# Optimization experiments

Measured on AMD Instinct MI355X. Metric: run time of the kernel, lower is better.

Reference implementation:

```python
import jax, jax.numpy as jnp
import numpy as np
from jax import lax

P = 2048
HIDDEN = 512
NUM_STEPS = 15
BATCH = 8192
SLOPE = 25.0  # snntorch surrogate.fast_sigmoid default slope


@jax.custom_vjp
def spike_fn(x):
    # Heaviside forward, fast-sigmoid surrogate backward.
    return (x > 0).astype(x.dtype)

def _spike_fwd(x):
    return spike_fn(x), x

def _spike_bwd(x, g):
    return (g / (SLOPE * jnp.abs(x) + 1.0) ** 2,)

spike_fn.defvjp(_spike_fwd, _spike_bwd)


def setup_inputs() -> dict:
    key = jax.random.key(0)
    ks = jax.random.split(key, 6)
    x = jax.random.randint(ks[0], (BATCH, 2), 0, P)
    embed = jax.random.normal(ks[1], (P, HIDDEN), dtype=jnp.float32)
    # Linear weights stored [in, out] (transpose of torch convention, same math)
    W1 = jax.random.normal(ks[2], (2 * HIDDEN, HIDDEN), dtype=jnp.float32) * (1.0 / np.sqrt(2 * HIDDEN))
    b1 = jnp.zeros((HIDDEN,), dtype=jnp.float32)
    W2 = jax.random.normal(ks[3], (HIDDEN, P), dtype=jnp.float32) * (1.0 / np.sqrt(HIDDEN))
    b2 = jnp.zeros((P,), dtype=jnp.float32)
    beta1 = jnp.float32(0.9)
    thr1 = jnp.float32(1.0)
    beta2 = jnp.float32(0.9)
    thr2 = jnp.float32(1.0)
    return {"x": x, "embed": embed, "W1": W1, "b1": b1, "W2": W2, "b2": b2,
            "beta1": beta1, "thr1": thr1, "beta2": beta2, "thr2": thr2}


def reference(x, embed, W1, b1, W2, b2, beta1, thr1, beta2, thr2):
    # clamp params as in the torch no-grad block (identity at init values)
    beta1 = jnp.clip(beta1, 0.1, 0.9)
    beta2 = jnp.clip(beta2, 0.1, 0.9)
    thr1 = jnp.clip(thr1, 0.1, None)
    thr2 = jnp.clip(thr2, 0.1, None)

    emb = embed[x].reshape(x.shape[0], -1)          # [B, 2*hidden]
    cur1 = emb @ W1 + b1                            # constant across steps

    mem1_0 = jnp.zeros((x.shape[0], HIDDEN), dtype=jnp.float32)
    mem2_0 = jnp.zeros((x.shape[0], P), dtype=jnp.float32)

    def step(carry, _):
        mem1, mem2 = carry
        # snntorch Leaky, reset_mechanism='subtract': reset from PREVIOUS mem, detached
        reset1 = lax.stop_gradient((mem1 - thr1 > 0).astype(mem1.dtype))
        mem1 = beta1 * mem1 + cur1 - reset1 * thr1
        spk1 = spike_fn(mem1 - thr1)
        cur2 = spk1 @ W2 + b2
        # lif2 has reset_mechanism='none'
        mem2 = beta2 * mem2 + cur2
        return (mem1, mem2), None

    (mem1, mem2), _ = lax.scan(step, (mem1_0, mem2_0), None, length=NUM_STEPS)
    return mem2  # output = last mem2
```

## Files before the change

### kernel.cpp

```cpp
#include <hip/hip_runtime.h>
#include <hip/hip_bf16.h>
#include <stdint.h>

typedef float    f32x4 __attribute__((ext_vector_type(4)));
typedef _Float16 f16x4 __attribute__((ext_vector_type(4)));
typedef _Float16 f16x8 __attribute__((ext_vector_type(8)));

#define NSTEPS 15

__global__ __launch_bounds__(256) void prep_kernel(
    const float* __restrict__ embed, const float* __restrict__ W1,
    const float* __restrict__ W2,
    _Float16* __restrict__ Ap, _Float16* __restrict__ Btp,
    _Float16* __restrict__ W2T)
{
  __shared__ _Float16 sh[2][64][72];
  const int b = blockIdx.x;
  const int t = threadIdx.x;

  if (b < 1024) {
    const int i  = b * 256 + t;
    const int m  = i >> 7;
    const int k4 = (i & 127) * 4;
    f32x4 v = *(const f32x4*)&embed[(size_t)m * 512 + k4];
    f16x4 h0, h1;
#pragma unroll
    for (int j = 0; j < 4; ++j) {
      h0[j] = (_Float16)v[j];
      h1[j] = (_Float16)(v[j] - (float)h0[j]);
    }
    _Float16* r = Ap + (size_t)m * 1024 + k4;
    *(f16x4*)(r)       = h0;
    *(f16x4*)(r + 512) = h1;
  } else if (b < 1152) {
    const int idx = b - 1024;
    const int n0 = (idx & 7) * 64;
    const int k0 = ((idx >> 3) & 7) * 64;
    const int z  = idx >> 6;
    const int kk = t >> 4;
    const int n4 = (t & 15) * 4;
#pragma unroll
    for (int i = 0; i < 4; ++i) {
      f32x4 v = *(const f32x4*)&W1[(size_t)(z * 512 + k0 + kk + i * 16) * 512 + n0 + n4];
#pragma unroll
      for (int j = 0; j < 4; ++j) {
        float s = v[j] * 64.0f;
        _Float16 hi = (_Float16)s;
        sh[0][n4 + j][kk + i * 16] = hi;
        sh[1][n4 + j][kk + i * 16] = (_Float16)(s - (float)hi);
      }
    }
    __syncthreads();
#pragma unroll
    for (int i = 0; i < 2; ++i) {
      const int nn = (t >> 3) + i * 32;
      const int k8 = (t & 7) * 8;
      _Float16* r = Btp + (size_t)(z * 512 + n0 + nn) * 1024 + k0 + k8;
      *(uint4*)(r)       = *(const uint4*)&sh[0][nn][k8];
      *(uint4*)(r + 512) = *(const uint4*)&sh[1][nn][k8];
    }
  } else {
    const int idx = b - 1152;
    const int n0 = (idx & 31) * 64;
    const int k0 = (idx >> 5) * 64;
    const int kk = t >> 4;
    const int n4 = (t & 15) * 4;
#pragma unroll
    for (int i = 0; i < 4; ++i) {
      f32x4 v = *(const f32x4*)&W2[(size_t)(k0 + kk + i * 16) * 2048 + n0 + n4];
#pragma unroll
      for (int j = 0; j < 4; ++j) sh[0][n4 + j][kk + i * 16] = (_Float16)v[j];
    }
    __syncthreads();
#pragma unroll
    for (int i = 0; i < 2; ++i) {
      const int nn = (t >> 3) + i * 32;
      const int k8 = (t & 7) * 8;
      *(uint4*)&W2T[(size_t)(n0 + nn) * 512 + k0 + k8] = *(const uint4*)&sh[0][nn][k8];
    }
  }
}

__device__ __forceinline__ void gld_lds16(const void* g, void* l) {
  __builtin_amdgcn_global_load_lds(
      (const __attribute__((address_space(1))) uint32_t*)g,
      (__attribute__((address_space(3))) uint32_t*)l, 16, 0, 0);
}

__global__ __launch_bounds__(256) void gemm1_kernel(
    const _Float16* __restrict__ Ap,
    const _Float16* __restrict__ Btp,
    float* __restrict__ T)
{
  __shared__ __align__(16) char lds[16384];
  char* AsB = lds;
  char* BsB = lds + 8192;

  const int t    = threadIdx.x;
  const int lane = t & 63;
  const int wave = t >> 6;
  const int wm   = wave >> 1;
  const int wn   = wave & 1;

  int bid = blockIdx.x;
  bid = (bid & 7) * 64 + (bid >> 3);
  const int m0 = (bid >> 4) * 64;
  const int n0 = (bid & 15) * 64;

  f32x4 acc[2][2] = {};

  for (int kt = 0; kt < 24; ++kt) {
    const int vk0  = kt * 64;
    const int acol = (vk0 < 1024) ? vk0 : vk0 - 1024;
    const int bcol = (vk0 < 1024) ? (vk0 & 511) : vk0 - 512;
#pragma unroll
    for (int i = 0; i < 2; ++i) {
      const int ob  = (wave * 2 + i) * 1024;
      const int o   = ob + lane * 16;
      const int row = o >> 7;
      const int c   = ((o >> 4) & 7) ^ (row & 7);
      gld_lds16(Ap + ((size_t)(m0 + row) * 1024 + acol + c * 8), AsB + ob);
    }
#pragma unroll
    for (int i = 0; i < 2; ++i) {
      const int ob  = (wave * 2 + i) * 1024;
      const int o   = ob + lane * 16;
      const int row = o >> 7;
      const int c   = ((o >> 4) & 7) ^ (row & 7);
      gld_lds16(Btp + ((size_t)(n0 + row) * 1024 + bcol + c * 8), BsB + ob);
    }
    asm volatile("s_waitcnt vmcnt(0)" ::: "memory");
    __syncthreads();

#pragma unroll
    for (int kk = 0; kk < 2; ++kk) {
      const int lc = (lane >> 4) + kk * 4;
      f16x8 af[2], bf[2];
#pragma unroll
      for (int mi = 0; mi < 2; ++mi) {
        const int row = wm * 32 + mi * 16 + (lane & 15);
        af[mi] = *(const f16x8*)(AsB + row * 128 + ((lc ^ (row & 7)) << 4));
      }
#pragma unroll
      for (int ni = 0; ni < 2; ++ni) {
        const int row = wn * 32 + ni * 16 + (lane & 15);
        bf[ni] = *(const f16x8*)(BsB + row * 128 + ((lc ^ (row & 7)) << 4));
      }
#pragma unroll
      for (int mi = 0; mi < 2; ++mi)
#pragma unroll
        for (int ni = 0; ni < 2; ++ni)
          acc[mi][ni] = __builtin_amdgcn_mfma_f32_16x16x32_f16(
              af[mi], bf[ni], acc[mi][ni], 0, 0, 0);
    }
    __syncthreads();
  }

#pragma unroll
  for (int mi = 0; mi < 2; ++mi) {
    const int r0 = m0 + wm * 32 + mi * 16 + ((lane >> 4) << 2);
#pragma unroll
    for (int ni = 0; ni < 2; ++ni) {
      const int cc = n0 + wn * 32 + ni * 16 + (lane & 15);
#pragma unroll
      for (int q = 0; q < 4; ++q)
        T[(size_t)(r0 + q) * 1024 + cc] = acc[mi][ni][q] * 0.015625f;
    }
  }
}

__global__ __launch_bounds__(256) void recur_kernel(
    const int* __restrict__ x,
    const float* __restrict__ T,
    const float* __restrict__ b1,
    const float* __restrict__ beta1p, const float* __restrict__ thr1p,
    const float* __restrict__ beta2p,
    _Float16* __restrict__ S)
{
  const float beta1 = fminf(fmaxf(beta1p[0], 0.1f), 0.9f);
  const float thr1  = fmaxf(thr1p[0], 0.1f);
  const float beta2 = fminf(fmaxf(beta2p[0], 0.1f), 0.9f);

  const int t = threadIdx.x;
  const int b = blockIdx.x * 4 + (t >> 6);
  const int h = (t & 63) * 8;
  const int x0 = x[b * 2 + 0];
  const int x1 = x[b * 2 + 1];

  const float* p0 = &T[(size_t)x0 * 1024 + h];
  const float* p1 = &T[(size_t)x1 * 1024 + 512 + h];

  float cur[8];
#pragma unroll
  for (int half = 0; half < 2; ++half) {
    f32x4 a = *(const f32x4*)(p0 + half * 4);
    f32x4 c = *(const f32x4*)(p1 + half * 4);
    f32x4 e = *(const f32x4*)&b1[h + half * 4];
#pragma unroll
    for (int j = 0; j < 4; ++j)
      cur[half * 4 + j] = (a[j] + c[j]) + e[j];
  }

  float m[8] = {}, s[8] = {};
#pragma unroll
  for (int st = 0; st < NSTEPS; ++st) {
#pragma unroll
    for (int j = 0; j < 8; ++j) {
      float r = (m[j] > thr1) ? thr1 : 0.0f;
      m[j] = beta1 * m[j] + cur[j] - r;
      float sp = (m[j] > thr1) ? 1.0f : 0.0f;
      s[j] = beta2 * s[j] + sp;
    }
  }

  __align__(16) _Float16 o[8];
#pragma unroll
  for (int j = 0; j < 8; ++j) o[j] = (_Float16)s[j];
  *(uint4*)&S[(size_t)b * 512 + h] = *(const uint4*)o;
}

__device__ __forceinline__ void g2_round(
    const _Float16* __restrict__ A, const _Float16* __restrict__ Bt,
    char* lds, int m0, int n0, int wave, int lane, int tile, int r)
{
  const int k0 = tile * 64;
  char* lb = lds + (tile % 3) * 49152;
  if (r < 4) {
    const int ob  = r * 8192 + wave * 1024;
    const int o   = ob + lane * 16;
    const int row = o >> 7;
    const int c   = ((o >> 4) & 7) ^ (row & 7);
    gld_lds16(A + ((size_t)(m0 + row) * 512 + k0 + c * 8), lb + ob);
  } else {
    const int ob  = (r - 4) * 8192 + wave * 1024;
    const int o   = ob + lane * 16;
    const int row = o >> 7;
    const int c   = ((o >> 4) & 7) ^ (row & 7);
    gld_lds16(Bt + ((size_t)(n0 + row) * 512 + k0 + c * 8), lb + 32768 + ob);
  }
}

template<int QA>
__device__ __forceinline__ void g2_mfma16(
    f32x4 (&acc)[8][2], const f16x8 (&af)[4][2], const f16x8 (&bf)[2][2])
{
#pragma unroll
  for (int kk = 0; kk < 2; ++kk)
#pragma unroll
    for (int mi = 0; mi < 4; ++mi)
#pragma unroll
      for (int ni = 0; ni < 2; ++ni)
        acc[QA * 4 + mi][ni] = __builtin_amdgcn_mfma_f32_16x16x32_f16(
            af[mi][kk], bf[ni][kk], acc[QA * 4 + mi][ni], 0, 0, 0);
}

template<int QA>
__device__ __forceinline__ void g2_lda(
    f16x8 (&af)[4][2], const char* lb, int wm, int lane)
{
#pragma unroll
  for (int mi = 0; mi < 4; ++mi) {
    const int row = wm * 128 + QA * 64 + mi * 16 + (lane & 15);
#pragma unroll
    for (int kk = 0; kk < 2; ++kk) {
      const int lc = (lane >> 4) + kk * 4;
      af[mi][kk] = *(const f16x8*)(lb + row * 128 + ((lc ^ (row & 7)) << 4));
    }
  }
}

__device__ __forceinline__ void g2_ldb(
    f16x8 (&bf)[2][2], const char* lb, int wn, int lane)
{
#pragma unroll
  for (int ni = 0; ni < 2; ++ni) {
    const int row = wn * 32 + ni * 16 + (lane & 15);
#pragma unroll
    for (int kk = 0; kk < 2; ++kk) {
      const int lc = (lane >> 4) + kk * 4;
      bf[ni][kk] = *(const f16x8*)(lb + 32768 + row * 128 + ((lc ^ (row & 7)) << 4));
    }
  }
}

__global__ __launch_bounds__(512, 2) void gemm2_pipe_kernel(
    const _Float16* __restrict__ A,
    const _Float16* __restrict__ Bt,
    const float* __restrict__ b2,
    const float* __restrict__ beta2p,
    float* __restrict__ C)
{
  __shared__ __align__(16) char lds[3 * 49152];

  const int t    = threadIdx.x;
  const int lane = t & 63;
  const int wave = t >> 6;
  const int wm   = wave >> 2;
  const int wn   = wave & 3;

  int bid = blockIdx.x;
  bid = (bid & 7) * 64 + (bid >> 3);
  const int m0 = (bid >> 4) * 256;
  const int n0 = (bid & 15) * 128;

  f32x4 acc[8][2] = {};
  f16x8 af[4][2], bf[2][2];

#pragma unroll
  for (int r = 0; r < 6; ++r) g2_round(A, Bt, lds, m0, n0, wave, lane, 0, r);
#pragma unroll
  for (int r = 0; r < 6; ++r) g2_round(A, Bt, lds, m0, n0, wave, lane, 1, r);
  asm volatile("s_waitcnt vmcnt(6)" ::: "memory");
  __builtin_amdgcn_s_barrier();

  for (int tt = 0; tt < 8; ++tt) {
    const char* lb = lds + (tt % 3) * 49152;
    const bool pf = (tt + 2 < 8);

    g2_lda<0>(af, lb, wm, lane);
    g2_ldb(bf, lb, wn, lane);
    if (pf) {
      g2_round(A, Bt, lds, m0, n0, wave, lane, tt + 2, 0);
      g2_round(A, Bt, lds, m0, n0, wave, lane, tt + 2, 1);
      g2_round(A, Bt, lds, m0, n0, wave, lane, tt + 2, 2);
    }
    __builtin_amdgcn_s_barrier();
    asm volatile("s_waitcnt lgkmcnt(0)" ::: "memory");
    __builtin_amdgcn_s_setprio(1);
    g2_mfma16<0>(acc, af, bf);
    __builtin_amdgcn_s_setprio(0);
    __builtin_amdgcn_s_barrier();

    g2_lda<1>(af, lb, wm, lane);
    if (pf) {
      g2_round(A, Bt, lds, m0, n0, wave, lane, tt + 2, 3);
      g2_round(A, Bt, lds, m0, n0, wave, lane, tt + 2, 4);
      g2_round(A, Bt, lds, m0, n0, wave, lane, tt + 2, 5);
    }
    __builtin_amdgcn_s_barrier();
    asm volatile("s_waitcnt lgkmcnt(0)" ::: "memory");
    __builtin_amdgcn_s_setprio(1);
    g2_mfma16<1>(acc, af, bf);
    __builtin_amdgcn_s_setprio(0);
    asm volatile("s_waitcnt vmcnt(6)" ::: "memory");
    __builtin_amdgcn_s_barrier();
  }

  const float beta2 = fminf(fmaxf(beta2p[0], 0.1f), 0.9f);
  float cb = 0.0f;
  for (int i = 0; i < NSTEPS; ++i) cb = beta2 * cb + 1.0f;

#pragma unroll
  for (int a = 0; a < 8; ++a) {
    const int r0 = m0 + wm * 128 + a * 16 + ((lane >> 4) << 2);
#pragma unroll
    for (int ni = 0; ni < 2; ++ni) {
      const int cc = n0 + wn * 32 + ni * 16 + (lane & 15);
      const float bv = cb * b2[cc];
#pragma unroll
      for (int q = 0; q < 4; ++q)
        C[(size_t)(r0 + q) * 2048 + cc] = acc[a][ni][q] + bv;
    }
  }
}

extern "C" void kernel_launch(void* const* d_in, const int* in_sizes, int n_in,
                              void* d_out, int out_size, void* d_ws, size_t ws_size,
                              hipStream_t stream) {
  const int*   x     = (const int*)  d_in[0];
  const float* embed = (const float*)d_in[1];
  const float* W1    = (const float*)d_in[2];
  const float* b1    = (const float*)d_in[3];
  const float* W2    = (const float*)d_in[4];
  const float* b2    = (const float*)d_in[5];
  const float* beta1 = (const float*)d_in[6];
  const float* thr1  = (const float*)d_in[7];
  const float* beta2 = (const float*)d_in[8];
  float* out = (float*)d_out;

  char* ws = (char*)d_ws;
  float*    T   = (float*)   ws;
  _Float16* Ap  = (_Float16*)(ws + ( 8u << 20));
  _Float16* Btp = (_Float16*)(ws + (12u << 20));
  _Float16* W2T = (_Float16*)(ws + (14u << 20));
  _Float16* S   = (_Float16*)(ws + (16u << 20));

  prep_kernel<<<dim3(1408), 256, 0, stream>>>(embed, W1, W2, Ap, Btp, W2T);

  gemm1_kernel<<<dim3(512), 256, 0, stream>>>(Ap, Btp, T);

  recur_kernel<<<dim3(2048), 256, 0, stream>>>(x, T, b1, beta1, thr1, beta2, S);

  gemm2_pipe_kernel<<<dim3(512), 512, 0, stream>>>(S, W2T, b2, beta2, out);
}
```

Measured before the change: 67.61 us.

## Triple-buffer gemm1 LDS tiles with two-ahead async prefetch

The gemm1 kernel moves from a single LDS buffer to a three-stage ring. Each iteration issues the global-to-LDS loads for tile kt+2 before running the MFMAs on tile kt, so memory latency overlaps with compute instead of stalling at a full vmcnt(0) wait every step. The LDS fragments are read into registers before the prefetch is issued, and MFMA issue priority is raised with s_setprio. The cost is three times the LDS per block (48KB), which can lower occupancy, and the partial vmcnt counting is fragile. gemm1 is only one of several kernels in the pipeline.

After: 64.42 us. 1.05x faster.

```diff
diff --git a/kernel.cpp b/kernel.cpp
--- a/kernel.cpp
+++ b/kernel.cpp
@@ -87,14 +87,38 @@
       (__attribute__((address_space(3))) uint32_t*)l, 16, 0, 0);
 }
 
+__device__ __forceinline__ void g1_stage(
+    const _Float16* __restrict__ Ap, const _Float16* __restrict__ Btp,
+    char* lds, int m0, int n0, int wave, int lane, int tile)
+{
+  const int vk0  = tile * 64;
+  const int acol = (vk0 < 1024) ? vk0 : vk0 - 1024;
+  const int bcol = (vk0 < 1024) ? (vk0 & 511) : vk0 - 512;
+  char* lb = lds + (tile % 3) * 16384;
+#pragma unroll
+  for (int i = 0; i < 2; ++i) {
+    const int ob  = (wave * 2 + i) * 1024;
+    const int o   = ob + lane * 16;
+    const int row = o >> 7;
+    const int c   = ((o >> 4) & 7) ^ (row & 7);
+    gld_lds16(Ap + ((size_t)(m0 + row) * 1024 + acol + c * 8), lb + ob);
+  }
+#pragma unroll
+  for (int i = 0; i < 2; ++i) {
+    const int ob  = (wave * 2 + i) * 1024;
+    const int o   = ob + lane * 16;
+    const int row = o >> 7;
+    const int c   = ((o >> 4) & 7) ^ (row & 7);
+    gld_lds16(Btp + ((size_t)(n0 + row) * 1024 + bcol + c * 8), lb + 8192 + ob);
+  }
+}
+
 __global__ __launch_bounds__(256) void gemm1_kernel(
     const _Float16* __restrict__ Ap,
     const _Float16* __restrict__ Btp,
     float* __restrict__ T)
 {
-  __shared__ __align__(16) char lds[16384];
-  char* AsB = lds;
-  char* BsB = lds + 8192;
+  __shared__ __align__(16) char lds[3 * 16384];
 
   const int t    = threadIdx.x;
   const int lane = t & 63;
@@ -109,51 +133,48 @@
 
   f32x4 acc[2][2] = {};
 
+  g1_stage(Ap, Btp, lds, m0, n0, wave, lane, 0);
+  g1_stage(Ap, Btp, lds, m0, n0, wave, lane, 1);
+  asm volatile("s_waitcnt vmcnt(4)" ::: "memory");
+  __builtin_amdgcn_s_barrier();
+
   for (int kt = 0; kt < 24; ++kt) {
-    const int vk0  = kt * 64;
-    const int acol = (vk0 < 1024) ? vk0 : vk0 - 1024;
-    const int bcol = (vk0 < 1024) ? (vk0 & 511) : vk0 - 512;
-#pragma unroll
-    for (int i = 0; i < 2; ++i) {
-      const int ob  = (wave * 2 + i) * 1024;
-      const int o   = ob + lane * 16;
-      const int row = o >> 7;
-      const int c   = ((o >> 4) & 7) ^ (row & 7);
-      gld_lds16(Ap + ((size_t)(m0 + row) * 1024 + acol + c * 8), AsB + ob);
-    }
-#pragma unroll
-    for (int i = 0; i < 2; ++i) {
-      const int ob  = (wave * 2 + i) * 1024;
-      const int o   = ob + lane * 16;
-      const int row = o >> 7;
-      const int c   = ((o >> 4) & 7) ^ (row & 7);
-      gld_lds16(Btp + ((size_t)(n0 + row) * 1024 + bcol + c * 8), BsB + ob);
-    }
-    asm volatile("s_waitcnt vmcnt(0)" ::: "memory");
-    __syncthreads();
-
+    const char* lb = lds + (kt % 3) * 16384;
+    char* AsB = (char*)lb;
+    char* BsB = (char*)lb + 8192;
+    const bool pf = (kt + 2 < 24);
+
+    f16x8 af[2][2], bf[2][2];
 #pragma unroll
     for (int kk = 0; kk < 2; ++kk) {
       const int lc = (lane >> 4) + kk * 4;
-      f16x8 af[2], bf[2];
 #pragma unroll
       for (int mi = 0; mi < 2; ++mi) {
         const int row = wm * 32 + mi * 16 + (lane & 15);
-        af[mi] = *(const f16x8*)(AsB + row * 128 + ((lc ^ (row & 7)) << 4));
+        af[mi][kk] = *(const f16x8*)(AsB + row * 128 + ((lc ^ (row & 7)) << 4));
       }
 #pragma unroll
       for (int ni = 0; ni < 2; ++ni) {
         const int row = wn * 32 + ni * 16 + (lane & 15);
-        bf[ni] = *(const f16x8*)(BsB + row * 128 + ((lc ^ (row & 7)) << 4));
+        bf[ni][kk] = *(const f16x8*)(BsB + row * 128 + ((lc ^ (row & 7)) << 4));
       }
+    }
+    if (pf) g1_stage(Ap, Btp, lds, m0, n0, wave, lane, kt + 2);
+
+    __builtin_amdgcn_s_setprio(1);
+#pragma unroll
+    for (int kk = 0; kk < 2; ++kk)
 #pragma unroll
       for (int mi = 0; mi < 2; ++mi)
 #pragma unroll
         for (int ni = 0; ni < 2; ++ni)
           acc[mi][ni] = __builtin_amdgcn_mfma_f32_16x16x32_f16(
-              af[mi], bf[ni], acc[mi][ni], 0, 0, 0);
-    }
-    __syncthreads();
+              af[mi][kk], bf[ni][kk], acc[mi][ni], 0, 0, 0);
+    __builtin_amdgcn_s_setprio(0);
+
+    if (pf) asm volatile("s_waitcnt vmcnt(4)" ::: "memory");
+    else    asm volatile("s_waitcnt vmcnt(0)" ::: "memory");
+    __builtin_amdgcn_s_barrier();
   }
 
 #pragma unroll
```
